# Performance work log

Hardware: AMD Instinct MI355X
Metric: run time of the kernel (lower is better)

The kernel has to match this reference:

```python
import jax, jax.numpy as jnp
import numpy as np

B, H, W, C = 64, 256, 256, 3  # batch, height, width, channels; choices dim is 2 (fake/real)


def setup_inputs() -> dict:
    key = jax.random.key(0)
    k1, k2, k3 = jax.random.split(key, 3)
    reals = jax.random.normal(k1, (B, H, W, C), dtype=jnp.float32)
    fakes = jax.random.normal(k2, (B, H, W, C), dtype=jnp.float32)
    shuffle_indices = jax.random.randint(k3, (B, 2), 0, 2).astype(jnp.int64)
    return {"reals": reals, "fakes": fakes, "shuffle_indices": shuffle_indices}


def reference(reals, fakes, shuffle_indices):
    # choice_images: (B, H, W, 2, C) -- fakes at choice index 0, reals at index 1
    choice_images = jnp.stack((fakes, reals), axis=-2)
    # Per-sample indices (B, 2) broadcast over H, W, C; single fused gather along
    # the choices axis replaces the original broadcast + tf.map_fn loop.
    idx = shuffle_indices.astype(jnp.int32)[:, None, None, :, None]  # (B,1,1,2,1)
    return jnp.take_along_axis(choice_images, idx, axis=-2)  # (B, H, W, 2, C)
```

## Files before the change

### kernel.cpp

```cpp
#include <hip/hip_runtime.h>


#define BB 64
#define HH 256
#define WW 256
#define HW (HH * WW)
#define PAIRS_PER_B (HW / 2)

__global__ __launch_bounds__(256) void tochoices_kernel(
    const float* __restrict__ reals,
    const float* __restrict__ fakes,
    const int* __restrict__ idx,
    float* __restrict__ out)
{
    int t = blockIdx.x * blockDim.x + threadIdx.x;
    int b  = t >> 15;
    int rp = t & (PAIRS_PER_B - 1);

    const float* s0 = idx[b * 2 + 0] ? reals : fakes;
    const float* s1 = idx[b * 2 + 1] ? reals : fakes;

    int pb = b * HW + rp * 2;

    const float2* p0 = (const float2*)(s0 + pb * 3);
    const float2* p1 = (const float2*)(s1 + pb * 3);
    float2 a01 = p0[0], a23 = p0[1], a45 = p0[2];
    float2 b01 = p1[0], b23 = p1[1], b45 = p1[2];

    float4* o = (float4*)(out + b * (HW * 6) + rp * 12);
    o[0] = make_float4(a01.x, a01.y, a23.x, b01.x);
    o[1] = make_float4(b01.y, b23.x, a23.y, a45.x);
    o[2] = make_float4(a45.y, b23.y, b45.x, b45.y);
}

extern "C" void kernel_launch(void* const* d_in, const int* in_sizes, int n_in,
                              void* d_out, int out_size, void* d_ws, size_t ws_size,
                              hipStream_t stream) {
    const float* reals = (const float*)d_in[0];
    const float* fakes = (const float*)d_in[1];
    const int*   idx   = (const int*)d_in[2];
    float* out = (float*)d_out;

    const int total_pairs = BB * PAIRS_PER_B;
    const int block = 256;
    const int grid = total_pairs / block;
    tochoices_kernel<<<grid, block, 0, stream>>>(reals, fakes, idx, out);
}
```

Baseline: 33.99 us.

## Stage input tiles in LDS with 16-byte loads and skip duplicate source read

Each block now loads a 1024-pixel tile of both selected sources into shared memory with float4 loads, then interleaves them into the output with coalesced float4 stores. When both indices pick the same source, the second tile is not loaded and the first is reused. This replaces strided float2 global loads with wider coalesced ones and cuts input traffic for duplicate choices, at the cost of LDS use, a barrier and fewer, larger blocks.

```diff
diff --git a/kernel.cpp b/kernel.cpp
--- a/kernel.cpp
+++ b/kernel.cpp
@@ -1,11 +1,13 @@
 #include <hip/hip_runtime.h>
 
 
-#define BB 64
-#define HH 256
-#define WW 256
-#define HW (HH * WW)
-#define PAIRS_PER_B (HW / 2)
+typedef float f32x4 __attribute__((ext_vector_type(4)));
+
+#define HW 65536
+#define TILE_PIX 1024
+#define TILES_PER_B (HW / TILE_PIX)
+#define SRC_FLOATS (TILE_PIX * 3)
+#define OUT_FLOATS (TILE_PIX * 6)
 
 __global__ __launch_bounds__(256) void tochoices_kernel(
     const float* __restrict__ reals,
@@ -13,24 +15,53 @@
     const int* __restrict__ idx,
     float* __restrict__ out)
 {
-    int t = blockIdx.x * blockDim.x + threadIdx.x;
-    int b  = t >> 15;
-    int rp = t & (PAIRS_PER_B - 1);
+    __shared__ __align__(16) float lds[SRC_FLOATS + 4 + SRC_FLOATS];
+    float* ldsA = lds;
+    float* ldsB = lds + SRC_FLOATS + 4;
 
-    const float* s0 = idx[b * 2 + 0] ? reals : fakes;
-    const float* s1 = idx[b * 2 + 1] ? reals : fakes;
+    int blk  = blockIdx.x;
+    int b    = blk >> 6;
+    int tile = blk & (TILES_PER_B - 1);
+    int t    = threadIdx.x;
 
-    int pb = b * HW + rp * 2;
+    int i0 = idx[b * 2 + 0];
+    int i1 = idx[b * 2 + 1];
 
-    const float2* p0 = (const float2*)(s0 + pb * 3);
-    const float2* p1 = (const float2*)(s1 + pb * 3);
-    float2 a01 = p0[0], a23 = p0[1], a45 = p0[2];
-    float2 b01 = p1[0], b23 = p1[1], b45 = p1[2];
+    long inbase = (long)b * (HW * 3) + (long)tile * SRC_FLOATS;
 
-    float4* o = (float4*)(out + b * (HW * 6) + rp * 12);
-    o[0] = make_float4(a01.x, a01.y, a23.x, b01.x);
-    o[1] = make_float4(b01.y, b23.x, a23.y, a45.x);
-    o[2] = make_float4(a45.y, b23.y, b45.x, b45.y);
+    const f32x4* pA = (const f32x4*)((i0 ? reals : fakes) + inbase);
+    #pragma unroll
+    for (int k = 0; k < 3; ++k)
+        ((f32x4*)ldsA)[t + 256 * k] = pA[t + 256 * k];
+
+    const float* B = ldsA;
+    if (i1 != i0) {
+        const f32x4* pB = (const f32x4*)((i1 ? reals : fakes) + inbase);
+        #pragma unroll
+        for (int k = 0; k < 3; ++k)
+            ((f32x4*)ldsB)[t + 256 * k] = pB[t + 256 * k];
+        B = ldsB;
+    }
+    __syncthreads();
+
+    f32x4* o = (f32x4*)(out + (long)b * (HW * 6) + (long)tile * OUT_FLOATS);
+    #pragma unroll
+    for (int k = 0; k < 6; ++k) {
+        int g = t + 256 * k;
+        int h = g / 3;
+        int r = g - 3 * h;
+        const float* a6 = ldsA + 6 * h;
+        const float* b6 = B    + 6 * h;
+
+        const float* px = (r == 0) ? a6 + 0 : (r == 1) ? b6 + 1 : a6 + 5;
+        const float* py = (r == 0) ? a6 + 1 : (r == 1) ? b6 + 2 : b6 + 3;
+        const float* pz = (r == 0) ? a6 + 2 : (r == 1) ? a6 + 3 : b6 + 4;
+        const float* pw = (r == 0) ? b6 + 0 : (r == 1) ? a6 + 4 : b6 + 5;
+
+        f32x4 v;
+        v.x = *px; v.y = *py; v.z = *pz; v.w = *pw;
+        o[g] = v;
+    }
 }
 
 extern "C" void kernel_launch(void* const* d_in, const int* in_sizes, int n_in,
@@ -41,8 +72,6 @@
     const int*   idx   = (const int*)d_in[2];
     float* out = (float*)d_out;
 
-    const int total_pairs = BB * PAIRS_PER_B;
-    const int block = 256;
-    const int grid = total_pairs / block;
-    tochoices_kernel<<<grid, block, 0, stream>>>(reals, fakes, idx, out);
+    const int grid = 64 * TILES_PER_B;
+    tochoices_kernel<<<grid, 256, 0, stream>>>(reals, fakes, idx, out);
 }
```

After: 30.83 us. 9.3% less time.

## Switch to scalar per-slot copies with grid-stride items per thread

Applied to the files above, without the earlier changes.

Each thread now copies four independent (pixel, slot) items of three floats each, using scalar loads and stores, instead of one pixel-pair with float2 loads and float4 stores. The items are strided by the total thread count, so consecutive threads touch adjacent 12-byte records and accesses stay coalesced, while the grid shrinks. The goal is more memory-level parallelism per thread and fewer blocks. The cost is narrower memory transactions and a per-item index lookup, which may lower effective bandwidth on this memory-bound copy.

```diff
diff --git a/kernel.cpp b/kernel.cpp
--- a/kernel.cpp
+++ b/kernel.cpp
@@ -1,11 +1,10 @@
 #include <hip/hip_runtime.h>
 
 
-#define BB 64
-#define HH 256
-#define WW 256
-#define HW (HH * WW)
-#define PAIRS_PER_B (HW / 2)
+#define HW 65536
+#define ITEMS (64 * HW * 2)
+#define ITEMS_PER_T 4
+#define TOTAL_T (ITEMS / ITEMS_PER_T)
 
 __global__ __launch_bounds__(256) void tochoices_kernel(
     const float* __restrict__ reals,
@@ -13,24 +12,22 @@
     const int* __restrict__ idx,
     float* __restrict__ out)
 {
-    int t = blockIdx.x * blockDim.x + threadIdx.x;
-    int b  = t >> 15;
-    int rp = t & (PAIRS_PER_B - 1);
+    int t0 = blockIdx.x * blockDim.x + threadIdx.x;
 
-    const float* s0 = idx[b * 2 + 0] ? reals : fakes;
-    const float* s1 = idx[b * 2 + 1] ? reals : fakes;
+    #pragma unroll
+    for (int k = 0; k < ITEMS_PER_T; ++k) {
+        int i    = t0 + k * TOTAL_T;
+        int b    = i >> 17;
+        int slot = i & 1;
+        int pix  = (i >> 1) & (HW - 1);
 
-    int pb = b * HW + rp * 2;
+        const float* s = idx[b * 2 + slot] ? reals : fakes;
+        const float* p = s + (b * HW + pix) * 3;
+        float x = p[0], y = p[1], z = p[2];
 
-    const float2* p0 = (const float2*)(s0 + pb * 3);
-    const float2* p1 = (const float2*)(s1 + pb * 3);
-    float2 a01 = p0[0], a23 = p0[1], a45 = p0[2];
-    float2 b01 = p1[0], b23 = p1[1], b45 = p1[2];
-
-    float4* o = (float4*)(out + b * (HW * 6) + rp * 12);
-    o[0] = make_float4(a01.x, a01.y, a23.x, b01.x);
-    o[1] = make_float4(b01.y, b23.x, a23.y, a45.x);
-    o[2] = make_float4(a45.y, b23.y, b45.x, b45.y);
+        float* o = out + (long)i * 3;
+        o[0] = x; o[1] = y; o[2] = z;
+    }
 }
 
 extern "C" void kernel_launch(void* const* d_in, const int* in_sizes, int n_in,
@@ -41,8 +38,7 @@
     const int*   idx   = (const int*)d_in[2];
     float* out = (float*)d_out;
 
-    const int total_pairs = BB * PAIRS_PER_B;
     const int block = 256;
-    const int grid = total_pairs / block;
+    const int grid = TOTAL_T / block;
     tochoices_kernel<<<grid, block, 0, stream>>>(reals, fakes, idx, out);
 }
```

Measured after the change: 31.19 us. -8.2%, faster.
